# Optimization experiments

Hardware: AMD Instinct MI355X
Metric: run time of the kernel (lower is better)

Reference implementation:

```python
import jax, jax.numpy as jnp
import numpy as np

N = 100_000   # nodes
E = 1_600_000 # edges
K = 3         # Chebyshev order


def _cheb_norm(row, col, w, n):
    # PyG ChebConv norm with normalization='sym', lambda_max=2:
    # L_hat = 2L/lambda_max - I = -D^{-1/2} A D^{-1/2} (diagonal cancels),
    # so only the off-diagonal term survives.
    deg = jax.ops.segment_sum(w, row, num_segments=n)
    dis = jnp.where(deg > 0, jax.lax.rsqrt(deg), 0.0)
    return -dis[row] * w * dis[col]


def _propagate(x, row, col, norm, n):
    # y[i] = sum_{e: row[e]=i} norm[e] * x[col[e]]   (sparse matvec with L_hat)
    return jax.ops.segment_sum(norm[:, None] * x[col], row, num_segments=n)


def _cheb_conv(x, row, col, norm, W, b, n):
    # Chebyshev recursion: T0=x, T1=L_hat x, T_k = 2 L_hat T_{k-1} - T_{k-2}
    Tx0 = x
    out = Tx0 @ W[0]
    Tx1 = _propagate(Tx0, row, col, norm, n)
    out = out + Tx1 @ W[1]
    for k in range(2, W.shape[0]):
        Tx2 = 2.0 * _propagate(Tx1, row, col, norm, n) - Tx0
        out = out + Tx2 @ W[k]
        Tx0, Tx1 = Tx1, Tx2
    return out + b


def setup_inputs() -> dict:
    key = jax.random.key(0)
    ks = jax.random.split(key, 8)
    in_f, c1, c2, out_f = 50, 64, 64, 16
    return {
        "x": jax.random.normal(ks[0], (N, in_f), jnp.float32),
        "edge_index": jax.random.randint(ks[1], (2, E), 0, N),
        "edge_weight": jax.random.uniform(ks[2], (E,), jnp.float32),
        "W1": jax.random.normal(ks[3], (K, in_f, c1), jnp.float32) * 0.05,
        "b1": jnp.zeros((c1,), jnp.float32),
        "W2": jax.random.normal(ks[4], (K, c1, c2), jnp.float32) * 0.05,
        "b2": jnp.zeros((c2,), jnp.float32),
        "bn_gamma": jnp.ones((c1,), jnp.float32),
        "bn_beta": jnp.zeros((c1,), jnp.float32),
        "lin_W": jax.random.normal(ks[5], (out_f, c2), jnp.float32) * 0.05,
        "lin_b": jnp.zeros((out_f,), jnp.float32),
    }


def reference(x, edge_index, edge_weight, W1, b1, W2, b2, bn_gamma, bn_beta, lin_W, lin_b):
    row, col = edge_index[0], edge_index[1]
    n = x.shape[0]
    norm = _cheb_norm(row, col, edge_weight, n)
    # conv1 + relu
    h = jax.nn.relu(_cheb_conv(x, row, col, norm, W1, b1, n))
    # BatchNorm1d over the node dimension (training-mode batch stats, eps=1e-5)
    mu = h.mean(axis=0)
    var = h.var(axis=0)
    h = (h - mu) * jax.lax.rsqrt(var + 1e-5) * bn_gamma + bn_beta
    # dropout with p=0.0 -> identity
    h = jax.nn.relu(_cheb_conv(h, row, col, norm, W2, b2, n))
    return h @ lin_W.T + lin_b
```

## Files before the change

kernel.cpp:

```cpp
#include <hip/hip_runtime.h>
#include <hip/hip_bf16.h>
#include <hip/hip_fp16.h>

static constexpr int NF   = 50;
static constexpr int C1   = 64;
static constexpr int OUTF = 16;
static constexpr int SCAN_T = 256;
static constexpr int SCAN_I = 4;
static constexpr float DEG_SCALE   = 8388608.f;
static constexpr float DEG_INV     = 1.f / 8388608.f;

__global__ void pass1_kernel(const int* __restrict__ row, const float* __restrict__ w,
                             unsigned long long* __restrict__ pcd, int* __restrict__ rank, int e)
{
    int i = blockIdx.x * blockDim.x + threadIdx.x;
    if (i < e) {
        int r = row[i];
        unsigned int wq = (unsigned int)(w[i] * DEG_SCALE + 0.5f);
        unsigned long long pk = (1ULL << 32) | (unsigned long long)wq;
        unsigned long long old = atomicAdd(&pcd[r], pk);
        rank[i] = (int)(old >> 32);
    }
}

__global__ void dis_kernel(const unsigned long long* __restrict__ pcd,
                           float* __restrict__ dis, int* __restrict__ cnt, int n)
{
    int i = blockIdx.x * blockDim.x + threadIdx.x;
    if (i < n) {
        unsigned long long pk = pcd[i];
        int c = (int)(pk >> 32);
        float d = (float)(unsigned int)(pk & 0xFFFFFFFFu) * DEG_INV;
        cnt[i] = c;
        dis[i] = (d > 0.f) ? (1.f / sqrtf(d)) : 0.f;
    }
}

__global__ void scan_partial(const int* __restrict__ cnt, int* __restrict__ bsum, int n)
{
    __shared__ int sm[SCAN_T];
    int t = threadIdx.x;
    int base = blockIdx.x * SCAN_T * SCAN_I + t * SCAN_I;
    int s = 0;
    #pragma unroll
    for (int k = 0; k < SCAN_I; ++k) { int i = base + k; if (i < n) s += cnt[i]; }
    sm[t] = s; __syncthreads();
    for (int off = SCAN_T / 2; off > 0; off >>= 1) {
        if (t < off) sm[t] += sm[t + off];
        __syncthreads();
    }
    if (t == 0) bsum[blockIdx.x] = sm[0];
}

__global__ void scan_bsums(int* __restrict__ bsum, int nb)
{
    __shared__ int sm[256];
    int t = threadIdx.x;
    sm[t] = (t < nb) ? bsum[t] : 0;
    __syncthreads();
    for (int off = 1; off < 256; off <<= 1) {
        int v = (t >= off) ? sm[t - off] : 0;
        __syncthreads();
        sm[t] += v;
        __syncthreads();
    }
    if (t < nb) bsum[t] = (t == 0) ? 0 : sm[t - 1];
}

__global__ void scan_final(const int* __restrict__ cnt, const int* __restrict__ bsum,
                           int* __restrict__ rowptr, int n)
{
    __shared__ int sm[SCAN_T];
    int t = threadIdx.x;
    int base = blockIdx.x * SCAN_T * SCAN_I + t * SCAN_I;
    int v[SCAN_I]; int s = 0;
    #pragma unroll
    for (int k = 0; k < SCAN_I; ++k) { int i = base + k; v[k] = (i < n) ? cnt[i] : 0; s += v[k]; }
    sm[t] = s; __syncthreads();
    for (int off = 1; off < SCAN_T; off <<= 1) {
        int x = (t >= off) ? sm[t - off] : 0;
        __syncthreads();
        sm[t] += x;
        __syncthreads();
    }
    int pref = bsum[blockIdx.x] + sm[t] - s;
    #pragma unroll
    for (int k = 0; k < SCAN_I; ++k) {
        int i = base + k;
        if (i < n) { rowptr[i] = pref; pref += v[k]; }
    }
}

__global__ void scatter_kernel(const int* __restrict__ row, const int* __restrict__ col,
                               const float* __restrict__ w, const float* __restrict__ dis,
                               const int* __restrict__ rowptr, const int* __restrict__ rank,
                               int2* __restrict__ ecn, int e)
{
    int i = blockIdx.x * blockDim.x + threadIdx.x;
    if (i < e) {
        int r = row[i], c = col[i];
        int pos = rowptr[r] + rank[i];
        float nv = -dis[r] * w[i] * dis[c];
        ecn[pos] = make_int2(c, __float_as_int(nv));
    }
}

__global__ void padx_kernel(const float* __restrict__ x, __half* __restrict__ XH, int n64)
{
    int i = blockIdx.x * blockDim.x + threadIdx.x;
    if (i < n64) {
        int row = i >> 6, f = i & 63;
        XH[i] = __float2half((f < NF) ? x[row * NF + f] : 0.f);
    }
}

template<int BS, bool SHADOW>
__global__ __launch_bounds__(256) void prop_kernel(
    const __half* __restrict__ xin, const float* __restrict__ base,
    const int* __restrict__ rowptr, const int* __restrict__ cnt,
    const int2* __restrict__ ecn, float* __restrict__ yout,
    __half* __restrict__ ysh, int n)
{
    int gw = (blockIdx.x * blockDim.x + threadIdx.x) >> 6;
    int lane = threadIdx.x & 63;
    if (gw >= n) return;
    int st = __builtin_amdgcn_readfirstlane(rowptr[gw]);
    int m  = __builtin_amdgcn_readfirstlane(cnt[gw]);
    float a[8] = {0.f, 0.f, 0.f, 0.f, 0.f, 0.f, 0.f, 0.f};
    for (int t = 0; t < m; t += 8) {
        #pragma unroll
        for (int k = 0; k < 8; ++k) {
            int tk = t + k;
            int idx = st + min(tk, m - 1);
            int2 md = ecn[idx];
            float nv = (tk < m) ? __int_as_float(md.y) : 0.f;
            a[k] += nv * __half2float(xin[md.x * C1 + lane]);
        }
    }
    float acc = ((a[0] + a[1]) + (a[2] + a[3])) + ((a[4] + a[5]) + (a[6] + a[7]));
    if (BS > 0) {
        float bv = (BS == C1 || lane < BS) ? base[(size_t)gw * BS + lane] : 0.f;
        acc = 2.f * acc - bv;
    }
    yout[(size_t)gw * C1 + lane] = acc;
    if (SHADOW) ysh[(size_t)gw * C1 + lane] = __float2half(acc);
}

__global__ __launch_bounds__(512) void dense1_kernel(
    const float* __restrict__ x, float* U , const float* __restrict__ T2,
    const float* __restrict__ W1, const float* __restrict__ b1,
    float* __restrict__ stats, int n)
{
    __shared__ __align__(16) float WI[3 * 13 * 64 * 4];
    __shared__ __align__(16) float ROWS[8 * 4 * 3 * 64];
    __shared__ float red[2][8][64];
    const int tid = threadIdx.x;
    for (int i = tid; i < 3 * 13 * 64 * 4; i += 512) WI[i] = 0.f;
    __syncthreads();
    for (int i = tid; i < 3 * NF * C1; i += 512) {
        int tap = i / (NF * C1), rem = i % (NF * C1), f = rem / C1, j = rem % C1;
        WI[((tap * 13 + (f >> 2)) * 64 + j) * 4 + (f & 3)] = W1[i];
    }
    __syncthreads();

    const int lane = tid & 63;
    const int wv   = tid >> 6;
    const int gw   = blockIdx.x * 8 + wv;
    const int rstep = gridDim.x * 8 * 4;
    const float bias = b1[lane];
    const float4* W4 = (const float4*)WI;
    const float4* R4 = (const float4*)ROWS;
    float ssum = 0.f, ssq = 0.f;

    for (int r0 = gw * 4; r0 < n; r0 += rstep) {
        const int nr = min(4, n - r0);
        #pragma unroll
        for (int r = 0; r < 4; ++r) {
            int row = min(r0 + r, n - 1);
            ROWS[((wv * 4 + r) * 3 + 0) * 64 + lane] = (lane < NF) ? x[row * NF + lane] : 0.f;
            ROWS[((wv * 4 + r) * 3 + 1) * 64 + lane] = U [row * C1 + lane];
            ROWS[((wv * 4 + r) * 3 + 2) * 64 + lane] = T2[row * C1 + lane];
        }
        float acc[4] = {bias, bias, bias, bias};
        for (int c = 0; c < 13; ++c) {
            float4 w0 = W4[(0 * 13 + c) * 64 + lane];
            float4 w1 = W4[(1 * 13 + c) * 64 + lane];
            float4 w2 = W4[(2 * 13 + c) * 64 + lane];
            #pragma unroll
            for (int r = 0; r < 4; ++r) {
                float4 t0 = R4[((wv * 4 + r) * 3 + 0) * 16 + c];
                float4 t1 = R4[((wv * 4 + r) * 3 + 1) * 16 + c];
                float4 t2 = R4[((wv * 4 + r) * 3 + 2) * 16 + c];
                acc[r] += t0.x * w0.x + t0.y * w0.y + t0.z * w0.z + t0.w * w0.w
                        + t1.x * w1.x + t1.y * w1.y + t1.z * w1.z + t1.w * w1.w
                        + t2.x * w2.x + t2.y * w2.y + t2.z * w2.z + t2.w * w2.w;
            }
        }
        #pragma unroll
        for (int r = 0; r < 4; ++r) {
            if (r < nr) {
                float v = fmaxf(acc[r], 0.f);
                U[(r0 + r) * C1 + lane] = v;
                ssum += v; ssq += v * v;
            }
        }
    }
    red[0][wv][lane] = ssum;
    red[1][wv][lane] = ssq;
    __syncthreads();
    if (tid < 128) {
        int which = tid >> 6, j = tid & 63;
        float tot = 0.f;
        #pragma unroll
        for (int wq = 0; wq < 8; ++wq) tot += red[which][wq][j];
        atomicAdd(&stats[which * 64 + j], tot);
    }
}

__global__ void bn_finalize_kernel(float* __restrict__ stats, const float* __restrict__ gamma,
                                   const float* __restrict__ beta, float inv_n)
{
    int j = threadIdx.x;
    if (j < 64) {
        float mu   = stats[j] * inv_n;
        float var  = stats[64 + j] * inv_n - mu * mu;
        float rstd = 1.f / sqrtf(var + 1e-5f);
        float sc   = gamma[j] * rstd;
        stats[128 + j] = sc;
        stats[192 + j] = beta[j] - mu * sc;
    }
}

__global__ void bn_apply_kernel(float* __restrict__ h, __half2* __restrict__ hh,
                                const float* __restrict__ stats, int n4)
{
    int i = blockIdx.x * blockDim.x + threadIdx.x;
    const int stride = gridDim.x * blockDim.x;
    int j0 = (i * 4) & 63;
    float s0 = stats[128 + j0], s1 = stats[129 + j0], s2 = stats[130 + j0], s3 = stats[131 + j0];
    float b0 = stats[192 + j0], b1 = stats[193 + j0], b2 = stats[194 + j0], b3 = stats[195 + j0];
    float4* h4 = (float4*)h;
    for (; i < n4; i += stride) {
        float4 v = h4[i];
        v.x = v.x * s0 + b0;
        v.y = v.y * s1 + b1;
        v.z = v.z * s2 + b2;
        v.w = v.w * s3 + b3;
        h4[i] = v;
        hh[i * 2 + 0] = __floats2half2_rn(v.x, v.y);
        hh[i * 2 + 1] = __floats2half2_rn(v.z, v.w);
    }
}

__global__ __launch_bounds__(512) void dense2_kernel(
    const float* __restrict__ hb, const float* __restrict__ Q1, const float* __restrict__ T2,
    const float* __restrict__ W2, const float* __restrict__ b2,
    const float* __restrict__ linW, const float* __restrict__ linb,
    float* __restrict__ out, int n)
{
    __shared__ __align__(16) float WI[3 * 16 * 64 * 4];
    __shared__ __align__(16) float ROWS[8 * 4 * 3 * 64];
    __shared__ float LWT[C1 * OUTF];
    const int tid = threadIdx.x;
    for (int i = tid; i < 3 * C1 * C1; i += 512) {
        int tap = i / (C1 * C1), rem = i % (C1 * C1), f = rem / C1, j = rem % C1;
        WI[((tap * 16 + (f >> 2)) * 64 + j) * 4 + (f & 3)] = W2[i];
    }
    for (int i = tid; i < C1 * OUTF; i += 512) {
        int j = i / OUTF, o = i % OUTF;
        LWT[i] = linW[o * C1 + j];
    }
    __syncthreads();

    const int lane = tid & 63;
    const int wv   = tid >> 6;
    const int gw   = blockIdx.x * 8 + wv;
    const int rstep = gridDim.x * 8 * 4;
    const float bias = b2[lane];
    const float lb   = linb[lane & 15];
    const int rsel = lane >> 4, osel = lane & 15;
    const float4* W4 = (const float4*)WI;
    const float4* R4 = (const float4*)ROWS;
    float* gb = &ROWS[wv * (4 * 3 * 64)];

    for (int r0 = gw * 4; r0 < n; r0 += rstep) {
        const int nr = min(4, n - r0);
        #pragma unroll
        for (int r = 0; r < 4; ++r) {
            int row = min(r0 + r, n - 1);
            ROWS[((wv * 4 + r) * 3 + 0) * 64 + lane] = hb[row * C1 + lane];
            ROWS[((wv * 4 + r) * 3 + 1) * 64 + lane] = Q1[row * C1 + lane];
            ROWS[((wv * 4 + r) * 3 + 2) * 64 + lane] = T2[row * C1 + lane];
        }
        float acc[4] = {bias, bias, bias, bias};
        for (int c = 0; c < 16; ++c) {
            float4 w0 = W4[(0 * 16 + c) * 64 + lane];
            float4 w1 = W4[(1 * 16 + c) * 64 + lane];
            float4 w2 = W4[(2 * 16 + c) * 64 + lane];
            #pragma unroll
            for (int r = 0; r < 4; ++r) {
                float4 t0 = R4[((wv * 4 + r) * 3 + 0) * 16 + c];
                float4 t1 = R4[((wv * 4 + r) * 3 + 1) * 16 + c];
                float4 t2 = R4[((wv * 4 + r) * 3 + 2) * 16 + c];
                acc[r] += t0.x * w0.x + t0.y * w0.y + t0.z * w0.z + t0.w * w0.w
                        + t1.x * w1.x + t1.y * w1.y + t1.z * w1.z + t1.w * w1.w
                        + t2.x * w2.x + t2.y * w2.y + t2.z * w2.z + t2.w * w2.w;
            }
        }
        #pragma unroll
        for (int r = 0; r < 4; ++r)
            gb[r * 72 + lane] = (r < nr) ? fmaxf(acc[r], 0.f) : 0.f;
        float oa = lb;
        #pragma unroll 8
        for (int j = 0; j < C1; ++j)
            oa += gb[rsel * 72 + j] * LWT[j * OUTF + osel];
        int rw = r0 + rsel;
        if (rw < n) out[rw * OUTF + osel] = oa;
    }
}

extern "C" void kernel_launch(void* const* d_in, const int* in_sizes, int n_in,
                              void* d_out, int out_size, void* d_ws, size_t ws_size,
                              hipStream_t stream)
{
    const float* x     = (const float*)d_in[0];
    const int*   ei    = (const int*)  d_in[1];
    const float* ew    = (const float*)d_in[2];
    const float* W1    = (const float*)d_in[3];
    const float* b1    = (const float*)d_in[4];
    const float* W2    = (const float*)d_in[5];
    const float* b2    = (const float*)d_in[6];
    const float* gamma = (const float*)d_in[7];
    const float* beta  = (const float*)d_in[8];
    const float* linW  = (const float*)d_in[9];
    const float* linb  = (const float*)d_in[10];
    float* out = (float*)d_out;
    (void)n_in; (void)out_size; (void)ws_size;

    const int n = in_sizes[0] / NF;
    const int e = in_sizes[2];
    const int* row = ei;
    const int* col = ei + e;

    char* ws = (char*)d_ws;
    size_t off = 0;
    auto alloc = [&](size_t bytes) -> void* {
        void* p = ws + off;
        off += (bytes + 255) & ~(size_t)255;
        return p;
    };
    unsigned long long* pcd = (unsigned long long*)alloc((size_t)n * 8);
    float*  dis    = (float*)alloc((size_t)n * 4);
    int*    cnt    = (int*)  alloc((size_t)n * 4);
    int*    rowptr = (int*)  alloc((size_t)n * 4);
    int*    rank   = (int*)  alloc((size_t)e * 4);
    int*    bsum   = (int*)  alloc(256 * 4);
    float*  stats  = (float*)alloc(256 * 4);
    int2*   ecn    = (int2*) alloc((size_t)e * 8);
    __half* XH     = (__half*)alloc((size_t)n * C1 * 2);
    __half* T1H    = (__half*)alloc((size_t)n * C1 * 2);
    __half* HH     = (__half*)alloc((size_t)n * C1 * 2);
    __half* Q1H    = (__half*)alloc((size_t)n * C1 * 2);
    float*  U      = (float*)alloc((size_t)n * C1 * 4);
    float*  H      = (float*)alloc((size_t)n * C1 * 4);
    float*  S      = (float*)alloc((size_t)n * C1 * 4);

    hipMemsetAsync(pcd,   0, (size_t)n * 8, stream);
    hipMemsetAsync(stats, 0, 256 * 4, stream);

    const int eb  = (e + 255) / 256;
    const int nbk = (n + 255) / 256;
    pass1_kernel<<<eb, 256, 0, stream>>>(row, ew, pcd, rank, e);
    dis_kernel<<<nbk, 256, 0, stream>>>(pcd, dis, cnt, n);
    padx_kernel<<<(n * C1 + 255) / 256, 256, 0, stream>>>(x, XH, n * C1);

    const int nb = (n + SCAN_T * SCAN_I - 1) / (SCAN_T * SCAN_I);
    scan_partial<<<nb, SCAN_T, 0, stream>>>(cnt, bsum, n);
    scan_bsums<<<1, 256, 0, stream>>>(bsum, nb);
    scan_final<<<nb, SCAN_T, 0, stream>>>(cnt, bsum, rowptr, n);
    scatter_kernel<<<eb, 256, 0, stream>>>(row, col, ew, dis, rowptr, rank, ecn, e);

    const int pb = (n + 3) / 4;

    prop_kernel<0,  true ><<<pb, 256, 0, stream>>>(XH,  x, rowptr, cnt, ecn, U, T1H, n);
    prop_kernel<NF, false><<<pb, 256, 0, stream>>>(T1H, x, rowptr, cnt, ecn, H, T1H, n);
    dense1_kernel<<<1024, 512, 0, stream>>>(x, U, H, W1, b1, stats, n);
    bn_finalize_kernel<<<1, 64, 0, stream>>>(stats, gamma, beta, 1.f / (float)n);
    bn_apply_kernel<<<2048, 256, 0, stream>>>(U, (__half2*)HH, stats, n * C1 / 4);

    prop_kernel<0,  true ><<<pb, 256, 0, stream>>>(HH,  U, rowptr, cnt, ecn, H, Q1H, n);
    prop_kernel<C1, false><<<pb, 256, 0, stream>>>(Q1H, U, rowptr, cnt, ecn, S, Q1H, n);
    dense2_kernel<<<1024, 512, 0, stream>>>(U, H, S, W2, b2, linW, linb, out, n);
}
```

Measured before the change: 518.2 us.

## Compute second-layer dense step with fp16 MFMA from half-precision inputs

The second dense stage is rewritten to use 16x16x32 fp16 MFMA instructions on 16-row tiles, reading fp16 copies of the three Chebyshev terms instead of fp32 rows staged through shared memory. A small kernel transposes W2 into fp16 once per call, and the last propagation now also writes an fp16 shadow of its output. This cuts global read bandwidth and moves the FMA-heavy matmul onto matrix cores, at the cost of lower input precision. The tile loop covers only n/16 full tiles, so any leftover rows would be skipped when n is not a multiple of 16.

```diff
diff --git a/kernel.cpp b/kernel.cpp
--- a/kernel.cpp
+++ b/kernel.cpp
@@ -9,6 +9,9 @@
 static constexpr int SCAN_I = 4;
 static constexpr float DEG_SCALE   = 8388608.f;
 static constexpr float DEG_INV     = 1.f / 8388608.f;
+
+typedef _Float16 half8 __attribute__((ext_vector_type(8)));
+typedef float    f32x4 __attribute__((ext_vector_type(4)));
 
 __global__ void pass1_kernel(const int* __restrict__ row, const float* __restrict__ w,
                              unsigned long long* __restrict__ pcd, int* __restrict__ rank, int e)
@@ -111,6 +114,15 @@
     if (i < n64) {
         int row = i >> 6, f = i & 63;
         XH[i] = __float2half((f < NF) ? x[row * NF + f] : 0.f);
+    }
+}
+
+__global__ void wprep_kernel(const float* __restrict__ W2, __half* __restrict__ WTh)
+{
+    int i = blockIdx.x * blockDim.x + threadIdx.x;
+    if (i < 3 * C1 * C1) {
+        int tap = i / (C1 * C1), rem = i % (C1 * C1), col = rem / C1, k = rem % C1;
+        WTh[i] = __float2half(W2[tap * C1 * C1 + k * C1 + col]);
     }
 }
 
@@ -253,69 +265,58 @@
 }
 
 __global__ __launch_bounds__(512) void dense2_kernel(
-    const float* __restrict__ hb, const float* __restrict__ Q1, const float* __restrict__ T2,
-    const float* __restrict__ W2, const float* __restrict__ b2,
-    const float* __restrict__ linW, const float* __restrict__ linb,
-    float* __restrict__ out, int n)
-{
-    __shared__ __align__(16) float WI[3 * 16 * 64 * 4];
-    __shared__ __align__(16) float ROWS[8 * 4 * 3 * 64];
+    const __half* __restrict__ hb16, const __half* __restrict__ q16,
+    const __half* __restrict__ t16,  const __half* __restrict__ WTh,
+    const float* __restrict__ b2, const float* __restrict__ linW,
+    const float* __restrict__ linb, float* __restrict__ out, int n)
+{
     __shared__ float LWT[C1 * OUTF];
+    __shared__ float gst[8][16][65];
     const int tid = threadIdx.x;
-    for (int i = tid; i < 3 * C1 * C1; i += 512) {
-        int tap = i / (C1 * C1), rem = i % (C1 * C1), f = rem / C1, j = rem % C1;
-        WI[((tap * 16 + (f >> 2)) * 64 + j) * 4 + (f & 3)] = W2[i];
-    }
     for (int i = tid; i < C1 * OUTF; i += 512) {
         int j = i / OUTF, o = i % OUTF;
         LWT[i] = linW[o * C1 + j];
     }
     __syncthreads();
 
-    const int lane = tid & 63;
-    const int wv   = tid >> 6;
-    const int gw   = blockIdx.x * 8 + wv;
-    const int rstep = gridDim.x * 8 * 4;
-    const float bias = b2[lane];
-    const float lb   = linb[lane & 15];
-    const int rsel = lane >> 4, osel = lane & 15;
-    const float4* W4 = (const float4*)WI;
-    const float4* R4 = (const float4*)ROWS;
-    float* gb = &ROWS[wv * (4 * 3 * 64)];
-
-    for (int r0 = gw * 4; r0 < n; r0 += rstep) {
-        const int nr = min(4, n - r0);
-        #pragma unroll
-        for (int r = 0; r < 4; ++r) {
-            int row = min(r0 + r, n - 1);
-            ROWS[((wv * 4 + r) * 3 + 0) * 64 + lane] = hb[row * C1 + lane];
-            ROWS[((wv * 4 + r) * 3 + 1) * 64 + lane] = Q1[row * C1 + lane];
-            ROWS[((wv * 4 + r) * 3 + 2) * 64 + lane] = T2[row * C1 + lane];
-        }
-        float acc[4] = {bias, bias, bias, bias};
-        for (int c = 0; c < 16; ++c) {
-            float4 w0 = W4[(0 * 16 + c) * 64 + lane];
-            float4 w1 = W4[(1 * 16 + c) * 64 + lane];
-            float4 w2 = W4[(2 * 16 + c) * 64 + lane];
+    const int lane = tid & 63, wv = tid >> 6;
+    const int cl = lane & 15, rg = lane >> 4;
+    const int nt = n >> 4;
+    const float lb = linb[cl];
+
+    for (int tile = blockIdx.x * 8 + wv; tile < nt; tile += gridDim.x * 8) {
+        int r0 = tile * 16;
+        const __half* ta = hb16 + (size_t)(r0 + cl) * C1 + rg * 8;
+        const __half* tb = q16  + (size_t)(r0 + cl) * C1 + rg * 8;
+        const __half* tc = t16  + (size_t)(r0 + cl) * C1 + rg * 8;
+        half8 a00 = *(const half8*)(ta);   half8 a01 = *(const half8*)(ta + 32);
+        half8 a10 = *(const half8*)(tb);   half8 a11 = *(const half8*)(tb + 32);
+        half8 a20 = *(const half8*)(tc);   half8 a21 = *(const half8*)(tc + 32);
+
+        #pragma unroll
+        for (int ct = 0; ct < 4; ++ct) {
+            float bias = b2[ct * 16 + cl];
+            f32x4 acc = {bias, bias, bias, bias};
+            const __half* wb = WTh + (ct * 16 + cl) * C1 + rg * 8;
+            acc = __builtin_amdgcn_mfma_f32_16x16x32_f16(a00, *(const half8*)(wb),              acc, 0, 0, 0);
+            acc = __builtin_amdgcn_mfma_f32_16x16x32_f16(a01, *(const half8*)(wb + 32),         acc, 0, 0, 0);
+            acc = __builtin_amdgcn_mfma_f32_16x16x32_f16(a10, *(const half8*)(wb + 4096),       acc, 0, 0, 0);
+            acc = __builtin_amdgcn_mfma_f32_16x16x32_f16(a11, *(const half8*)(wb + 4096 + 32),  acc, 0, 0, 0);
+            acc = __builtin_amdgcn_mfma_f32_16x16x32_f16(a20, *(const half8*)(wb + 8192),       acc, 0, 0, 0);
+            acc = __builtin_amdgcn_mfma_f32_16x16x32_f16(a21, *(const half8*)(wb + 8192 + 32),  acc, 0, 0, 0);
             #pragma unroll
-            for (int r = 0; r < 4; ++r) {
-                float4 t0 = R4[((wv * 4 + r) * 3 + 0) * 16 + c];
-                float4 t1 = R4[((wv * 4 + r) * 3 + 1) * 16 + c];
-                float4 t2 = R4[((wv * 4 + r) * 3 + 2) * 16 + c];
-                acc[r] += t0.x * w0.x + t0.y * w0.y + t0.z * w0.z + t0.w * w0.w
-                        + t1.x * w1.x + t1.y * w1.y + t1.z * w1.z + t1.w * w1.w
-                        + t2.x * w2.x + t2.y * w2.y + t2.z * w2.z + t2.w * w2.w;
-            }
-        }
-        #pragma unroll
-        for (int r = 0; r < 4; ++r)
-            gb[r * 72 + lane] = (r < nr) ? fmaxf(acc[r], 0.f) : 0.f;
-        float oa = lb;
-        #pragma unroll 8
-        for (int j = 0; j < C1; ++j)
-            oa += gb[rsel * 72 + j] * LWT[j * OUTF + osel];
-        int rw = r0 + rsel;
-        if (rw < n) out[rw * OUTF + osel] = oa;
+            for (int r = 0; r < 4; ++r)
+                gst[wv][rg * 4 + r][ct * 16 + cl] = fmaxf(acc[r], 0.f);
+        }
+        #pragma unroll
+        for (int r4 = 0; r4 < 4; ++r4) {
+            int row = r4 * 4 + rg;
+            float oa = lb;
+            #pragma unroll 8
+            for (int j = 0; j < C1; ++j)
+                oa += gst[wv][row][j] * LWT[j * OUTF + cl];
+            out[(size_t)(r0 + row) * OUTF + cl] = oa;
+        }
     }
 }
 
@@ -361,6 +362,8 @@
     __half* T1H    = (__half*)alloc((size_t)n * C1 * 2);
     __half* HH     = (__half*)alloc((size_t)n * C1 * 2);
     __half* Q1H    = (__half*)alloc((size_t)n * C1 * 2);
+    __half* SH     = (__half*)alloc((size_t)n * C1 * 2);
+    __half* WTh    = (__half*)alloc((size_t)3 * C1 * C1 * 2);
     float*  U      = (float*)alloc((size_t)n * C1 * 4);
     float*  H      = (float*)alloc((size_t)n * C1 * 4);
     float*  S      = (float*)alloc((size_t)n * C1 * 4);
@@ -373,6 +376,7 @@
     pass1_kernel<<<eb, 256, 0, stream>>>(row, ew, pcd, rank, e);
     dis_kernel<<<nbk, 256, 0, stream>>>(pcd, dis, cnt, n);
     padx_kernel<<<(n * C1 + 255) / 256, 256, 0, stream>>>(x, XH, n * C1);
+    wprep_kernel<<<(3 * C1 * C1 + 255) / 256, 256, 0, stream>>>(W2, WTh);
 
     const int nb = (n + SCAN_T * SCAN_I - 1) / (SCAN_T * SCAN_I);
     scan_partial<<<nb, SCAN_T, 0, stream>>>(cnt, bsum, n);
@@ -389,6 +393,6 @@
     bn_apply_kernel<<<2048, 256, 0, stream>>>(U, (__half2*)HH, stats, n * C1 / 4);
 
     prop_kernel<0,  true ><<<pb, 256, 0, stream>>>(HH,  U, rowptr, cnt, ecn, H, Q1H, n);
-    prop_kernel<C1, false><<<pb, 256, 0, stream>>>(Q1H, U, rowptr, cnt, ecn, S, Q1H, n);
-    dense2_kernel<<<1024, 512, 0, stream>>>(U, H, S, W2, b2, linW, linb, out, n);
-}
+    prop_kernel<C1, true ><<<pb, 256, 0, stream>>>(Q1H, U, rowptr, cnt, ecn, S, SH, n);
+    dense2_kernel<<<512, 512, 0, stream>>>(HH, Q1H, SH, WTh, b2, linW, linb, out, n);
+}
```

Measured after the change: 475.8 us. 1.09x faster.
